# Kernel optimization log

Hardware: AMD Instinct MI355X
Metric: run time of the kernel (lower is better)

The kernel has to match this reference:

```python
import jax, jax.numpy as jnp
import numpy as np

N = 2048  # device_num
K = 32    # neighbors per device


def setup_inputs() -> dict:
    key = jax.random.key(0)
    k1, k2, k3 = jax.random.split(key, 3)
    dynamic_re = jax.random.uniform(k1, (N, N), dtype=jnp.float32)
    static_re = jax.random.uniform(k2, (N,), dtype=jnp.float32)
    # neighbor ids in [0, N) excluding self (draw in [0, N-1) then shift past row index)
    r = jax.random.randint(k3, (N, K), 0, N - 1)
    rows = jnp.arange(N)[:, None]
    neighbor_matrix = (r + (r >= rows)).astype(jnp.int32)
    return {"dynamic_re": dynamic_re, "static_re": static_re, "neighbor_matrix": neighbor_matrix}


def _trust_forward(dynamic_re, static_re, neighbor_matrix):
    # Semantics of RobustTrustComputing.__call__ on a fresh instance (temp_storage empty):
    #  - diagonal: 1.0
    #  - neighbor (j in nbr(i)): history has len 1 -> CI branch is False -> combined
    #    tau = 0.7*dyn[i,j] + 0.3*stat[j]; prev==combined -> hysteresis takes the
    #    'x <= prev' path: sigmoid(combined + 0.5) with sigmoid(z)=(1-e^-z)/(1+e^-z)=tanh(z/2)
    #  - non-neighbor with common neighbors c: 0.8 * mean_c rep[i,c]*rep[c,j] read from the
    #    PARTIALLY-FILLED matrix in row-major write order (rep[i,c] nonzero only if c<j,
    #    rep[c,j] nonzero only if c<i); divisor is the FULL common-neighbor count.
    #  - non-neighbor, no common neighbors: 0.5*stat[j]
    #  - final clamp to [0,1]
    n = dynamic_re.shape[0]
    idx = jnp.arange(n)
    # membership matrix: M[i, c] True iff c appears in neighbor list of i
    M = jnp.zeros((n, n), dtype=bool).at[idx[:, None], neighbor_matrix].set(True)
    nbrval = jnp.tanh(0.5 * (0.7 * dynamic_re + 0.3 * static_re[None, :] + 0.5))
    Mf = M.astype(dynamic_re.dtype)
    count = Mf @ Mf.T                                  # |common neighbors(i, j)|
    Bmask = Mf.T * (idx[:, None] < idx[None, :])       # [c, j]: c in nbr(j) AND c < j
    fallback = 0.5 * static_re                         # [j]

    def step(rep, xs):
        i, M_i, nbr_i, cnt_i = xs
        # rep[i, c] (c in nbr(i)) equals nbrval[i, c] once column c has been written (c < j,
        # handled by Bmask); rep[c, j] is the final row c only for c < i (rows >= i are zero).
        A = jnp.where(M_i & (idx < i), nbr_i, 0.0)     # [c]
        num = jnp.einsum('c,cj,cj->j', A, rep, Bmask)  # [j]
        indirect = 0.8 * num / jnp.maximum(cnt_i, 1.0)
        row = jnp.where(M_i, nbr_i, jnp.where(cnt_i > 0, indirect, fallback))
        row = jnp.where(idx == i, 1.0, row)            # diagonal overrides everything
        return rep.at[i].set(row), None

    rep0 = jnp.zeros((n, n), dynamic_re.dtype)
    rep, _ = jax.lax.scan(step, rep0, (idx, M, nbrval, count))
    return jnp.clip(rep, 0.0, 1.0)


def reference(dynamic_re, static_re, neighbor_matrix):
    return _trust_forward(dynamic_re, static_re, neighbor_matrix)
```

## Files before the change

### kernel.cpp

```cpp
#include <hip/hip_runtime.h>
#include <math.h>
#include <limits.h>

#define WAVE 64
#define KMAX 32
#define IMAX 96

__device__ __forceinline__ float nvval(float d, float s) {
    return tanhf(0.5f * (0.7f * d + 0.3f * s + 0.5f));
}
__device__ __forceinline__ float clamp01(float x) {
    return fminf(fmaxf(x, 0.0f), 1.0f);
}

__global__ void build_lists(const int* __restrict__ nbr, int N, int K, int W,
                            int* __restrict__ nbrs_sorted, int* __restrict__ deg,
                            unsigned* __restrict__ Mbits, unsigned* __restrict__ Tbits,
                            int* __restrict__ invcnt, int* __restrict__ invlist,
                            int* __restrict__ invpos) {
    int tid = blockIdx.x * blockDim.x + threadIdx.x;
    int i = tid / WAVE;
    int lane = tid % WAVE;
    if (i >= N) return;
    bool have = (lane < K);
    int val = have ? nbr[(size_t)i * K + lane] : INT_MAX;
    bool dup = false;
    for (int t = 0; t < K; ++t) {
        int vt = __shfl(val, t);
        if (have && t < lane && vt == val) dup = true;
    }
    int dupi = (dup || !have) ? 1 : 0;
    int pos = 0;
    for (int t = 0; t < K; ++t) {
        int vt = __shfl(val, t);
        int dt = __shfl(dupi, t);
        if (!dt && vt < val) pos++;
    }
    int myp = (have && !dup) ? pos : -1;
    unsigned long long m = __ballot(have && !dup);
    int degv = __popcll(m);
    int slot = INT_MAX;
    for (int t = 0; t < K; ++t) {
        int pt = __shfl(myp, t);
        int vt = __shfl(val, t);
        if (pt == lane) slot = vt;
    }
    if (lane < K) nbrs_sorted[(size_t)i * K + lane] = slot;
    if (lane == 0) deg[i] = degv;
    if (have) {
        atomicOr(&Mbits[(size_t)i * W + (val >> 5)], 1u << (val & 31));
        atomicOr(&Tbits[(size_t)val * W + (i >> 5)], 1u << (i & 31));
        if (!dup) {
            int p = atomicAdd(&invcnt[val], 1);
            if (p < IMAX) invlist[(size_t)val * IMAX + p] = i;
            invpos[(size_t)i * K + myp] = p;
        }
    }
}

__global__ void __launch_bounds__(256) phase1(
        const float* __restrict__ dyn, const float* __restrict__ stat,
        const int* __restrict__ nbrs_sorted, const int* __restrict__ deg,
        const unsigned* __restrict__ Mbits, const unsigned* __restrict__ Tbits,
        const int* __restrict__ invpos, int N, int K, int W,
        float* __restrict__ Vcomp) {
    __shared__ float s_nv[4 * KMAX * KMAX];
    int tid = blockIdx.x * blockDim.x + threadIdx.x;
    int j = tid / WAVE;
    int lane = threadIdx.x & (WAVE - 1);
    int waveid = threadIdx.x >> 6;
    if (j >= N) return;
    int degj = deg[j];
    int c = (lane < K) ? nbrs_sorted[(size_t)j * K + lane] : INT_MAX;
    bool validk = (lane < degj);
    float sk = validk ? stat[c] : 0.0f;
    float statj = stat[j];
    float* s_row = &s_nv[waveid * KMAX * KMAX];

    unsigned dirbit = 0;
    if (validk) {
        unsigned w = Tbits[(size_t)j * W + (c >> 5)];
        dirbit = (w >> (c & 31)) & 1u;
    }
    unsigned dirmask = (unsigned)__ballot(dirbit != 0);
    float dv = 0.0f;
    if (dirbit) dv = nvval(dyn[(size_t)c * N + j], statj);

    unsigned hmAll = 0;
    #pragma unroll
    for (int m = 0; m < KMAX; ++m) {
        int cm = __shfl(c, m);
        if (cm < N) {
            unsigned w = validk ? Mbits[(size_t)cm * W + (c >> 5)] : 0u;
            unsigned b = (w >> (c & 31)) & 1u;
            hmAll |= b << m;
            if (b && lane < m && c < j)
                s_row[m * KMAX + lane] = nvval(dyn[(size_t)cm * N + c], sk);
        }
    }
    unsigned lm = (lane < 31) ? (0xFFFFFFFEu << lane) : 0u;
    unsigned hmTerm = (validk && c < j) ? (hmAll & lm) : 0u;

    int mycnt = 0;
    unsigned H = 0;
    #pragma unroll
    for (int m = 0; m < KMAX; ++m) {
        unsigned long long ball = __ballot((hmAll >> m) & 1u);
        unsigned long long ballT = __ballot((hmTerm >> m) & 1u);
        if (lane == m) mycnt = __popcll(ball);
        H |= (ballT ? 1u : 0u) << m;
    }
    H = __builtin_amdgcn_readfirstlane(H);
    dirmask = __builtin_amdgcn_readfirstlane(dirmask);

    float v = 0.0f;
    #pragma unroll
    for (int m = 0; m < KMAX; ++m) {
        float num = 0.0f;
        if (H & (1u << m)) {
            float t = 0.0f;
            if ((hmTerm >> m) & 1u) t = s_row[m * KMAX + lane] * v;
            num = t;
            num += __shfl_xor(num, 16);
            num += __shfl_xor(num, 8);
            num += __shfl_xor(num, 4);
            num += __shfl_xor(num, 2);
            num += __shfl_xor(num, 1);
        }
        float val;
        if ((dirmask >> m) & 1u) val = dv;
        else if (mycnt > 0) val = 0.8f * num / (float)mycnt;
        else val = 0.5f * statj;
        val = clamp01(val);
        if (lane == m) v = val;
    }
    if (validk) {
        int p = invpos[(size_t)j * K + lane];
        if (p < IMAX) Vcomp[(size_t)c * IMAX + p] = v;
    }
}

__global__ void __launch_bounds__(256) phase2(
        const float* __restrict__ dyn, const float* __restrict__ stat,
        const int* __restrict__ nbrs_sorted,
        const int* __restrict__ invcnt, const int* __restrict__ invlist,
        const float* __restrict__ Vcomp,
        int N, int K, float* __restrict__ out) {
    extern __shared__ char smem[];
    int* s_cnt = (int*)smem;
    float* s_num = (float*)(s_cnt + N);
    int* s_nbr = (int*)(s_num + N);
    float* s_nv = (float*)(s_nbr + K);
    int* s_icnt = (int*)(s_nv + K);
    __shared__ int s_me;

    int i = blockIdx.x;
    int tid = threadIdx.x;

    for (int t = tid; t < N; t += blockDim.x) { s_cnt[t] = 0; s_num[t] = 0.0f; }
    if (tid < K) {
        int c = nbrs_sorted[(size_t)i * K + tid];
        s_nbr[tid] = c;
        if (c < N) {
            s_nv[tid] = nvval(dyn[(size_t)i * N + c], stat[c]);
            int m = invcnt[c];
            s_icnt[tid] = (m < IMAX) ? m : IMAX;
        } else {
            s_nv[tid] = 0.0f;
            s_icnt[tid] = 0;
        }
    }
    if (tid == 0) {
        int m = invcnt[i];
        s_me = (m < IMAX) ? m : IMAX;
    }
    __syncthreads();

    {
        int k = tid >> 3;
        int e0 = tid & 7;
        if (k < K) {
            int c = s_nbr[k];
            int m = s_icnt[k];
            float nv = s_nv[k];
            if (c < N) {
                for (int e = e0; e < m; e += 8) {
                    int j = invlist[(size_t)c * IMAX + e];
                    atomicAdd(&s_cnt[j], 1);
                    if (c < i && c < j)
                        atomicAdd(&s_num[j], nv * Vcomp[(size_t)c * IMAX + e]);
                }
            }
        }
    }
    __syncthreads();

    if (tid < K) {
        int c = s_nbr[tid];
        if (c < N) { s_cnt[c] = -1; s_num[c] = s_nv[tid]; }
    }
    __syncthreads();

    for (int e = tid; e < s_me; e += blockDim.x) {
        int j = invlist[(size_t)i * IMAX + e];
        s_cnt[j] = -1;
        s_num[j] = Vcomp[(size_t)i * IMAX + e];
    }
    __syncthreads();

    for (int j = tid; j < N; j += blockDim.x) {
        int cnt = s_cnt[j];
        float val;
        if (j == i) val = 1.0f;
        else if (cnt < 0) val = s_num[j];
        else if (cnt > 0) val = 0.8f * s_num[j] / (float)cnt;
        else val = 0.5f * stat[j];
        out[(size_t)i * N + j] = clamp01(val);
    }
}

extern "C" void kernel_launch(void* const* d_in, const int* in_sizes, int n_in,
                              void* d_out, int out_size, void* d_ws, size_t ws_size,
                              hipStream_t stream) {
    const float* dyn = (const float*)d_in[0];
    const float* stat = (const float*)d_in[1];
    const int* nbr = (const int*)d_in[2];
    int N = in_sizes[1];
    int K = in_sizes[2] / N;
    int W = (N + 31) / 32;
    float* out = (float*)d_out;

    char* ws = (char*)d_ws;
    size_t offNbr = 0;
    size_t offDeg = offNbr + (size_t)N * K * sizeof(int);
    size_t offM = offDeg + (size_t)N * sizeof(int);
    size_t offT = offM + (size_t)N * W * sizeof(unsigned);
    size_t offIC = offT + (size_t)N * W * sizeof(unsigned);
    size_t offIP = offIC + (size_t)N * sizeof(int);
    size_t offIL = offIP + (size_t)N * K * sizeof(int);
    size_t offVC = offIL + (size_t)N * IMAX * sizeof(int);
    int* nbrs_sorted = (int*)(ws + offNbr);
    int* deg = (int*)(ws + offDeg);
    unsigned* Mbits = (unsigned*)(ws + offM);
    unsigned* Tbits = (unsigned*)(ws + offT);
    int* invcnt = (int*)(ws + offIC);
    int* invpos = (int*)(ws + offIP);
    int* invlist = (int*)(ws + offIL);
    float* Vcomp = (float*)(ws + offVC);

    hipMemsetAsync(ws + offM, 0, offIP - offM, stream);

    int threads = 256;
    int blocksWave = (N * WAVE + threads - 1) / threads;
    build_lists<<<blocksWave, threads, 0, stream>>>(nbr, N, K, W, nbrs_sorted, deg,
                                                    Mbits, Tbits, invcnt, invlist,
                                                    invpos);
    phase1<<<blocksWave, threads, 0, stream>>>(dyn, stat, nbrs_sorted, deg,
                                               Mbits, Tbits, invpos, N, K, W, Vcomp);
    size_t smem = (size_t)N * 8 + (size_t)K * 12 + 16;
    phase2<<<N, threads, smem, stream>>>(dyn, stat, nbrs_sorted,
                                         invcnt, invlist, Vcomp, N, K, out);
}
```

Measured before the change: 125.0 us.

## Fuse three kernels into one persistent kernel with software grid barriers

Replaces the build_lists, phase1 and phase2 launches, plus the large memset, with a single persistent kernel of 512 blocks. It zeroes the bitmaps in-kernel and separates the phases with atomic-counter grid barriers. Each block handles 4 rows per phase, so launch gaps and inter-kernel idle time go away. In exchange the kernel depends on all 512 blocks being co-resident (launch bounds allow 2 per CU) to avoid deadlock. Phase 2 also has less parallelism, because each block now processes 4 rows in sequence instead of one block per row.

```diff
diff --git a/kernel.cpp b/kernel.cpp
--- a/kernel.cpp
+++ b/kernel.cpp
@@ -5,6 +5,8 @@
 #define WAVE 64
 #define KMAX 32
 #define IMAX 96
+#define NBLK 512
+#define TPB  256
 
 __device__ __forceinline__ float nvval(float d, float s) {
     return tanhf(0.5f * (0.7f * d + 0.3f * s + 0.5f));
@@ -13,209 +15,226 @@
     return fminf(fmaxf(x, 0.0f), 1.0f);
 }
 
-__global__ void build_lists(const int* __restrict__ nbr, int N, int K, int W,
-                            int* __restrict__ nbrs_sorted, int* __restrict__ deg,
-                            unsigned* __restrict__ Mbits, unsigned* __restrict__ Tbits,
-                            int* __restrict__ invcnt, int* __restrict__ invlist,
-                            int* __restrict__ invpos) {
-    int tid = blockIdx.x * blockDim.x + threadIdx.x;
-    int i = tid / WAVE;
-    int lane = tid % WAVE;
-    if (i >= N) return;
-    bool have = (lane < K);
-    int val = have ? nbr[(size_t)i * K + lane] : INT_MAX;
-    bool dup = false;
-    for (int t = 0; t < K; ++t) {
-        int vt = __shfl(val, t);
-        if (have && t < lane && vt == val) dup = true;
-    }
-    int dupi = (dup || !have) ? 1 : 0;
-    int pos = 0;
-    for (int t = 0; t < K; ++t) {
-        int vt = __shfl(val, t);
-        int dt = __shfl(dupi, t);
-        if (!dt && vt < val) pos++;
-    }
-    int myp = (have && !dup) ? pos : -1;
-    unsigned long long m = __ballot(have && !dup);
-    int degv = __popcll(m);
-    int slot = INT_MAX;
-    for (int t = 0; t < K; ++t) {
-        int pt = __shfl(myp, t);
-        int vt = __shfl(val, t);
-        if (pt == lane) slot = vt;
-    }
-    if (lane < K) nbrs_sorted[(size_t)i * K + lane] = slot;
-    if (lane == 0) deg[i] = degv;
-    if (have) {
-        atomicOr(&Mbits[(size_t)i * W + (val >> 5)], 1u << (val & 31));
-        atomicOr(&Tbits[(size_t)val * W + (i >> 5)], 1u << (i & 31));
-        if (!dup) {
-            int p = atomicAdd(&invcnt[val], 1);
-            if (p < IMAX) invlist[(size_t)val * IMAX + p] = i;
-            invpos[(size_t)i * K + myp] = p;
-        }
-    }
-}
-
-__global__ void __launch_bounds__(256) phase1(
+__device__ __forceinline__ void grid_sync(unsigned* bar) {
+    __threadfence();
+    __syncthreads();
+    if (threadIdx.x == 0) {
+        __hip_atomic_fetch_add(bar, 1u, __ATOMIC_ACQ_REL, __HIP_MEMORY_SCOPE_AGENT);
+        while (__hip_atomic_load(bar, __ATOMIC_ACQUIRE, __HIP_MEMORY_SCOPE_AGENT) < (unsigned)NBLK)
+            __builtin_amdgcn_s_sleep(8);
+    }
+    __syncthreads();
+    __threadfence();
+}
+
+__global__ void __launch_bounds__(TPB, 2) fused(
         const float* __restrict__ dyn, const float* __restrict__ stat,
-        const int* __restrict__ nbrs_sorted, const int* __restrict__ deg,
-        const unsigned* __restrict__ Mbits, const unsigned* __restrict__ Tbits,
-        const int* __restrict__ invpos, int N, int K, int W,
-        float* __restrict__ Vcomp) {
-    __shared__ float s_nv[4 * KMAX * KMAX];
-    int tid = blockIdx.x * blockDim.x + threadIdx.x;
-    int j = tid / WAVE;
-    int lane = threadIdx.x & (WAVE - 1);
-    int waveid = threadIdx.x >> 6;
-    if (j >= N) return;
-    int degj = deg[j];
-    int c = (lane < K) ? nbrs_sorted[(size_t)j * K + lane] : INT_MAX;
-    bool validk = (lane < degj);
-    float sk = validk ? stat[c] : 0.0f;
-    float statj = stat[j];
-    float* s_row = &s_nv[waveid * KMAX * KMAX];
-
-    unsigned dirbit = 0;
-    if (validk) {
-        unsigned w = Tbits[(size_t)j * W + (c >> 5)];
-        dirbit = (w >> (c & 31)) & 1u;
-    }
-    unsigned dirmask = (unsigned)__ballot(dirbit != 0);
-    float dv = 0.0f;
-    if (dirbit) dv = nvval(dyn[(size_t)c * N + j], statj);
-
-    unsigned hmAll = 0;
-    #pragma unroll
-    for (int m = 0; m < KMAX; ++m) {
-        int cm = __shfl(c, m);
-        if (cm < N) {
-            unsigned w = validk ? Mbits[(size_t)cm * W + (c >> 5)] : 0u;
-            unsigned b = (w >> (c & 31)) & 1u;
-            hmAll |= b << m;
-            if (b && lane < m && c < j)
-                s_row[m * KMAX + lane] = nvval(dyn[(size_t)cm * N + c], sk);
-        }
-    }
-    unsigned lm = (lane < 31) ? (0xFFFFFFFEu << lane) : 0u;
-    unsigned hmTerm = (validk && c < j) ? (hmAll & lm) : 0u;
-
-    int mycnt = 0;
-    unsigned H = 0;
-    #pragma unroll
-    for (int m = 0; m < KMAX; ++m) {
-        unsigned long long ball = __ballot((hmAll >> m) & 1u);
-        unsigned long long ballT = __ballot((hmTerm >> m) & 1u);
-        if (lane == m) mycnt = __popcll(ball);
-        H |= (ballT ? 1u : 0u) << m;
-    }
-    H = __builtin_amdgcn_readfirstlane(H);
-    dirmask = __builtin_amdgcn_readfirstlane(dirmask);
-
-    float v = 0.0f;
-    #pragma unroll
-    for (int m = 0; m < KMAX; ++m) {
-        float num = 0.0f;
-        if (H & (1u << m)) {
-            float t = 0.0f;
-            if ((hmTerm >> m) & 1u) t = s_row[m * KMAX + lane] * v;
-            num = t;
-            num += __shfl_xor(num, 16);
-            num += __shfl_xor(num, 8);
-            num += __shfl_xor(num, 4);
-            num += __shfl_xor(num, 2);
-            num += __shfl_xor(num, 1);
-        }
-        float val;
-        if ((dirmask >> m) & 1u) val = dv;
-        else if (mycnt > 0) val = 0.8f * num / (float)mycnt;
-        else val = 0.5f * statj;
-        val = clamp01(val);
-        if (lane == m) v = val;
-    }
-    if (validk) {
-        int p = invpos[(size_t)j * K + lane];
-        if (p < IMAX) Vcomp[(size_t)c * IMAX + p] = v;
-    }
-}
-
-__global__ void __launch_bounds__(256) phase2(
-        const float* __restrict__ dyn, const float* __restrict__ stat,
-        const int* __restrict__ nbrs_sorted,
-        const int* __restrict__ invcnt, const int* __restrict__ invlist,
-        const float* __restrict__ Vcomp,
-        int N, int K, float* __restrict__ out) {
-    extern __shared__ char smem[];
-    int* s_cnt = (int*)smem;
-    float* s_num = (float*)(s_cnt + N);
-    int* s_nbr = (int*)(s_num + N);
-    float* s_nv = (float*)(s_nbr + K);
-    int* s_icnt = (int*)(s_nv + K);
-    __shared__ int s_me;
-
-    int i = blockIdx.x;
+        const int* __restrict__ nbr, int N, int K, int W,
+        unsigned* __restrict__ Mbits, unsigned* __restrict__ Tbits,
+        int* __restrict__ invcnt, unsigned* __restrict__ bars,
+        int* __restrict__ invpos, int* __restrict__ invlist,
+        float* __restrict__ Vcomp, int* __restrict__ nbrs_sorted,
+        int* __restrict__ deg, float* __restrict__ out) {
+    __shared__ __align__(16) char smem[17 * 1024];
     int tid = threadIdx.x;
-
-    for (int t = tid; t < N; t += blockDim.x) { s_cnt[t] = 0; s_num[t] = 0.0f; }
-    if (tid < K) {
-        int c = nbrs_sorted[(size_t)i * K + tid];
-        s_nbr[tid] = c;
-        if (c < N) {
-            s_nv[tid] = nvval(dyn[(size_t)i * N + c], stat[c]);
-            int m = invcnt[c];
-            s_icnt[tid] = (m < IMAX) ? m : IMAX;
-        } else {
-            s_nv[tid] = 0.0f;
-            s_icnt[tid] = 0;
-        }
-    }
-    if (tid == 0) {
-        int m = invcnt[i];
-        s_me = (m < IMAX) ? m : IMAX;
-    }
-    __syncthreads();
+    int lane = tid & (WAVE - 1);
+    int wid = tid >> 6;
+    int row = blockIdx.x * 4 + wid;
 
     {
-        int k = tid >> 3;
-        int e0 = tid & 7;
-        if (k < K) {
-            int c = s_nbr[k];
-            int m = s_icnt[k];
-            float nv = s_nv[k];
-            if (c < N) {
-                for (int e = e0; e < m; e += 8) {
-                    int j = invlist[(size_t)c * IMAX + e];
-                    atomicAdd(&s_cnt[j], 1);
-                    if (c < i && c < j)
-                        atomicAdd(&s_num[j], nv * Vcomp[(size_t)c * IMAX + e]);
+        size_t zwords = (size_t)N * W * 2 + N;
+        unsigned* zb = Mbits;
+        for (size_t t = (size_t)blockIdx.x * TPB + tid; t < zwords; t += (size_t)NBLK * TPB)
+            zb[t] = 0u;
+    }
+    grid_sync(&bars[0]);
+
+    if (row < N) {
+        int i = row;
+        bool have = (lane < K);
+        int val = have ? nbr[(size_t)i * K + lane] : INT_MAX;
+        bool dup = false;
+        for (int t = 0; t < KMAX; ++t) {
+            int vt = __shfl(val, t);
+            if (have && t < lane && vt == val) dup = true;
+        }
+        int dupi = (dup || !have) ? 1 : 0;
+        int pos = 0;
+        for (int t = 0; t < KMAX; ++t) {
+            int vt = __shfl(val, t);
+            int dt = __shfl(dupi, t);
+            if (!dt && vt < val) pos++;
+        }
+        int myp = (have && !dup) ? pos : -1;
+        unsigned long long m = __ballot(have && !dup);
+        int degv = __popcll(m);
+        int slot = INT_MAX;
+        for (int t = 0; t < KMAX; ++t) {
+            int pt = __shfl(myp, t);
+            int vt = __shfl(val, t);
+            if (pt == lane) slot = vt;
+        }
+        if (lane < K) nbrs_sorted[(size_t)i * K + lane] = slot;
+        if (lane == 0) deg[i] = degv;
+        if (have) {
+            atomicOr(&Mbits[(size_t)i * W + (val >> 5)], 1u << (val & 31));
+            atomicOr(&Tbits[(size_t)val * W + (i >> 5)], 1u << (i & 31));
+            if (!dup) {
+                int p = atomicAdd(&invcnt[val], 1);
+                if (p < IMAX) invlist[(size_t)val * IMAX + p] = i;
+                invpos[(size_t)i * K + myp] = p;
+            }
+        }
+    }
+    grid_sync(&bars[1]);
+
+    if (row < N) {
+        int j = row;
+        float* s_row = (float*)smem + (size_t)wid * KMAX * KMAX;
+        int degj = deg[j];
+        int c = (lane < K) ? nbrs_sorted[(size_t)j * K + lane] : INT_MAX;
+        bool validk = (lane < degj);
+        float sk = validk ? stat[c] : 0.0f;
+        float statj = stat[j];
+
+        unsigned dirbit = 0;
+        if (validk) {
+            unsigned w = Tbits[(size_t)j * W + (c >> 5)];
+            dirbit = (w >> (c & 31)) & 1u;
+        }
+        unsigned dirmask = (unsigned)__ballot(dirbit != 0);
+        float dv = 0.0f;
+        if (dirbit) dv = nvval(dyn[(size_t)c * N + j], statj);
+
+        unsigned hmAll = 0;
+        #pragma unroll
+        for (int m = 0; m < KMAX; ++m) {
+            int cm = __shfl(c, m);
+            if (cm < N) {
+                unsigned w = validk ? Mbits[(size_t)cm * W + (c >> 5)] : 0u;
+                unsigned b = (w >> (c & 31)) & 1u;
+                hmAll |= b << m;
+                if (b && lane < m && c < j)
+                    s_row[m * KMAX + lane] = nvval(dyn[(size_t)cm * N + c], sk);
+            }
+        }
+        unsigned lm = (lane < 31) ? (0xFFFFFFFEu << lane) : 0u;
+        unsigned hmTerm = (validk && c < j) ? (hmAll & lm) : 0u;
+
+        int mycnt = 0;
+        unsigned H = 0;
+        #pragma unroll
+        for (int m = 0; m < KMAX; ++m) {
+            unsigned long long ball = __ballot((hmAll >> m) & 1u);
+            unsigned long long ballT = __ballot((hmTerm >> m) & 1u);
+            if (lane == m) mycnt = __popcll(ball);
+            H |= (ballT ? 1u : 0u) << m;
+        }
+        H = __builtin_amdgcn_readfirstlane(H);
+        dirmask = __builtin_amdgcn_readfirstlane(dirmask);
+
+        float v = 0.0f;
+        #pragma unroll
+        for (int m = 0; m < KMAX; ++m) {
+            float num = 0.0f;
+            if (H & (1u << m)) {
+                float t = 0.0f;
+                if ((hmTerm >> m) & 1u) t = s_row[m * KMAX + lane] * v;
+                num = t;
+                num += __shfl_xor(num, 16);
+                num += __shfl_xor(num, 8);
+                num += __shfl_xor(num, 4);
+                num += __shfl_xor(num, 2);
+                num += __shfl_xor(num, 1);
+            }
+            float val;
+            if ((dirmask >> m) & 1u) val = dv;
+            else if (mycnt > 0) val = 0.8f * num / (float)mycnt;
+            else val = 0.5f * statj;
+            val = clamp01(val);
+            if (lane == m) v = val;
+        }
+        if (validk) {
+            int p = invpos[(size_t)j * K + lane];
+            if (p < IMAX) Vcomp[(size_t)c * IMAX + p] = v;
+        }
+    }
+    grid_sync(&bars[2]);
+
+    {
+        int* s_cnt = (int*)smem;
+        float* s_num = (float*)(s_cnt + N);
+        int* s_nbr = (int*)(s_num + N);
+        float* s_nv = (float*)(s_nbr + KMAX);
+        int* s_icnt = (int*)(s_nv + KMAX);
+        int* s_me = (int*)(s_icnt + KMAX);
+
+        for (int r = 0; r < 4; ++r) {
+            int i = blockIdx.x * 4 + r;
+            if (i >= N) break;
+            __syncthreads();
+            for (int t = tid; t < N; t += TPB) { s_cnt[t] = 0; s_num[t] = 0.0f; }
+            if (tid < K) {
+                int c = nbrs_sorted[(size_t)i * K + tid];
+                s_nbr[tid] = c;
+                if (c < N) {
+                    s_nv[tid] = nvval(dyn[(size_t)i * N + c], stat[c]);
+                    int m = invcnt[c];
+                    s_icnt[tid] = (m < IMAX) ? m : IMAX;
+                } else {
+                    s_nv[tid] = 0.0f;
+                    s_icnt[tid] = 0;
                 }
             }
-        }
-    }
-    __syncthreads();
-
-    if (tid < K) {
-        int c = s_nbr[tid];
-        if (c < N) { s_cnt[c] = -1; s_num[c] = s_nv[tid]; }
-    }
-    __syncthreads();
-
-    for (int e = tid; e < s_me; e += blockDim.x) {
-        int j = invlist[(size_t)i * IMAX + e];
-        s_cnt[j] = -1;
-        s_num[j] = Vcomp[(size_t)i * IMAX + e];
-    }
-    __syncthreads();
-
-    for (int j = tid; j < N; j += blockDim.x) {
-        int cnt = s_cnt[j];
-        float val;
-        if (j == i) val = 1.0f;
-        else if (cnt < 0) val = s_num[j];
-        else if (cnt > 0) val = 0.8f * s_num[j] / (float)cnt;
-        else val = 0.5f * stat[j];
-        out[(size_t)i * N + j] = clamp01(val);
+            if (tid == 0) {
+                int m = invcnt[i];
+                *s_me = (m < IMAX) ? m : IMAX;
+            }
+            __syncthreads();
+
+            {
+                int k = tid >> 3;
+                int e0 = tid & 7;
+                if (k < K) {
+                    int c = s_nbr[k];
+                    int m = s_icnt[k];
+                    float nv = s_nv[k];
+                    if (c < N) {
+                        for (int e = e0; e < m; e += 8) {
+                            int j = invlist[(size_t)c * IMAX + e];
+                            atomicAdd(&s_cnt[j], 1);
+                            if (c < i && c < j)
+                                atomicAdd(&s_num[j], nv * Vcomp[(size_t)c * IMAX + e]);
+                        }
+                    }
+                }
+            }
+            __syncthreads();
+
+            if (tid < K) {
+                int c = s_nbr[tid];
+                if (c < N) { s_cnt[c] = -1; s_num[c] = s_nv[tid]; }
+            }
+            __syncthreads();
+
+            int me = *s_me;
+            for (int e = tid; e < me; e += TPB) {
+                int j = invlist[(size_t)i * IMAX + e];
+                s_cnt[j] = -1;
+                s_num[j] = Vcomp[(size_t)i * IMAX + e];
+            }
+            __syncthreads();
+
+            for (int j = tid; j < N; j += TPB) {
+                int cnt = s_cnt[j];
+                float val;
+                if (j == i) val = 1.0f;
+                else if (cnt < 0) val = s_num[j];
+                else if (cnt > 0) val = 0.8f * s_num[j] / (float)cnt;
+                else val = 0.5f * stat[j];
+                out[(size_t)i * N + j] = clamp01(val);
+            }
+        }
     }
 }
 
@@ -231,33 +250,28 @@
     float* out = (float*)d_out;
 
     char* ws = (char*)d_ws;
-    size_t offNbr = 0;
-    size_t offDeg = offNbr + (size_t)N * K * sizeof(int);
-    size_t offM = offDeg + (size_t)N * sizeof(int);
+    size_t offM = 0;
     size_t offT = offM + (size_t)N * W * sizeof(unsigned);
     size_t offIC = offT + (size_t)N * W * sizeof(unsigned);
-    size_t offIP = offIC + (size_t)N * sizeof(int);
+    size_t offBar = offIC + (size_t)N * sizeof(int);
+    size_t offIP = offBar + 64;
     size_t offIL = offIP + (size_t)N * K * sizeof(int);
     size_t offVC = offIL + (size_t)N * IMAX * sizeof(int);
-    int* nbrs_sorted = (int*)(ws + offNbr);
-    int* deg = (int*)(ws + offDeg);
+    size_t offNbr = offVC + (size_t)N * IMAX * sizeof(float);
+    size_t offDeg = offNbr + (size_t)N * K * sizeof(int);
     unsigned* Mbits = (unsigned*)(ws + offM);
     unsigned* Tbits = (unsigned*)(ws + offT);
     int* invcnt = (int*)(ws + offIC);
+    unsigned* bars = (unsigned*)(ws + offBar);
     int* invpos = (int*)(ws + offIP);
     int* invlist = (int*)(ws + offIL);
     float* Vcomp = (float*)(ws + offVC);
-
-    hipMemsetAsync(ws + offM, 0, offIP - offM, stream);
-
-    int threads = 256;
-    int blocksWave = (N * WAVE + threads - 1) / threads;
-    build_lists<<<blocksWave, threads, 0, stream>>>(nbr, N, K, W, nbrs_sorted, deg,
-                                                    Mbits, Tbits, invcnt, invlist,
-                                                    invpos);
-    phase1<<<blocksWave, threads, 0, stream>>>(dyn, stat, nbrs_sorted, deg,
-                                               Mbits, Tbits, invpos, N, K, W, Vcomp);
-    size_t smem = (size_t)N * 8 + (size_t)K * 12 + 16;
-    phase2<<<N, threads, smem, stream>>>(dyn, stat, nbrs_sorted,
-                                         invcnt, invlist, Vcomp, N, K, out);
-}
+    int* nbrs_sorted = (int*)(ws + offNbr);
+    int* deg = (int*)(ws + offDeg);
+
+    hipMemsetAsync(ws + offBar, 0, 64, stream);
+
+    fused<<<NBLK, TPB, 0, stream>>>(dyn, stat, nbr, N, K, W,
+                                    Mbits, Tbits, invcnt, bars,
+                                    invpos, invlist, Vcomp, nbrs_sorted, deg, out);
+}
```

Result: slower. 429.4 us (+243.6%).

## Drop transposed bitmask, build membership bits without atomics, vectorize phase2 reads

Applied to the files above, without the earlier changes.

Removes the Tbits transposed membership bitmap. Phase1 now tests direct membership by reading Mbits[c] at bit j. Each lane builds one Mbits word from wave shuffles and writes it directly, which removes the global atomicOr traffic and shrinks the workspace memset to just invcnt. Phase2 reads the inverse lists and Vcomp with int4/float4 loads, and tanh is replaced by an exp-based formula. The lane-per-word Mbits build assumes W fits in one 64-lane wave (N ≤ 2048), and the fast exp path slightly changes numerics.

```diff
diff --git a/kernel.cpp b/kernel.cpp
--- a/kernel.cpp
+++ b/kernel.cpp
@@ -7,7 +7,9 @@
 #define IMAX 96
 
 __device__ __forceinline__ float nvval(float d, float s) {
-    return tanhf(0.5f * (0.7f * d + 0.3f * s + 0.5f));
+    float z = 0.7f * d + 0.3f * s + 0.5f;
+    float e = __expf(z);
+    return 1.0f - 2.0f / (e + 1.0f);
 }
 __device__ __forceinline__ float clamp01(float x) {
     return fminf(fmaxf(x, 0.0f), 1.0f);
@@ -15,7 +17,7 @@
 
 __global__ void build_lists(const int* __restrict__ nbr, int N, int K, int W,
                             int* __restrict__ nbrs_sorted, int* __restrict__ deg,
-                            unsigned* __restrict__ Mbits, unsigned* __restrict__ Tbits,
+                            unsigned* __restrict__ Mbits,
                             int* __restrict__ invcnt, int* __restrict__ invlist,
                             int* __restrict__ invpos) {
     int tid = blockIdx.x * blockDim.x + threadIdx.x;
@@ -25,13 +27,18 @@
     bool have = (lane < K);
     int val = have ? nbr[(size_t)i * K + lane] : INT_MAX;
     bool dup = false;
-    for (int t = 0; t < K; ++t) {
+    unsigned mybits = 0;
+    #pragma unroll
+    for (int t = 0; t < KMAX; ++t) {
         int vt = __shfl(val, t);
         if (have && t < lane && vt == val) dup = true;
-    }
+        if ((vt >> 5) == lane) mybits |= 1u << (vt & 31);
+    }
+    if (lane < W) Mbits[(size_t)i * W + lane] = mybits;
     int dupi = (dup || !have) ? 1 : 0;
     int pos = 0;
-    for (int t = 0; t < K; ++t) {
+    #pragma unroll
+    for (int t = 0; t < KMAX; ++t) {
         int vt = __shfl(val, t);
         int dt = __shfl(dupi, t);
         if (!dt && vt < val) pos++;
@@ -40,28 +47,25 @@
     unsigned long long m = __ballot(have && !dup);
     int degv = __popcll(m);
     int slot = INT_MAX;
-    for (int t = 0; t < K; ++t) {
+    #pragma unroll
+    for (int t = 0; t < KMAX; ++t) {
         int pt = __shfl(myp, t);
         int vt = __shfl(val, t);
         if (pt == lane) slot = vt;
     }
     if (lane < K) nbrs_sorted[(size_t)i * K + lane] = slot;
     if (lane == 0) deg[i] = degv;
-    if (have) {
-        atomicOr(&Mbits[(size_t)i * W + (val >> 5)], 1u << (val & 31));
-        atomicOr(&Tbits[(size_t)val * W + (i >> 5)], 1u << (i & 31));
-        if (!dup) {
-            int p = atomicAdd(&invcnt[val], 1);
-            if (p < IMAX) invlist[(size_t)val * IMAX + p] = i;
-            invpos[(size_t)i * K + myp] = p;
-        }
+    if (have && !dup) {
+        int p = atomicAdd(&invcnt[val], 1);
+        if (p < IMAX) invlist[(size_t)val * IMAX + p] = i;
+        invpos[(size_t)i * K + myp] = p;
     }
 }
 
 __global__ void __launch_bounds__(256) phase1(
         const float* __restrict__ dyn, const float* __restrict__ stat,
         const int* __restrict__ nbrs_sorted, const int* __restrict__ deg,
-        const unsigned* __restrict__ Mbits, const unsigned* __restrict__ Tbits,
+        const unsigned* __restrict__ Mbits,
         const int* __restrict__ invpos, int N, int K, int W,
         float* __restrict__ Vcomp) {
     __shared__ float s_nv[4 * KMAX * KMAX];
@@ -79,8 +83,8 @@
 
     unsigned dirbit = 0;
     if (validk) {
-        unsigned w = Tbits[(size_t)j * W + (c >> 5)];
-        dirbit = (w >> (c & 31)) & 1u;
+        unsigned w = Mbits[(size_t)c * W + (j >> 5)];
+        dirbit = (w >> (j & 31)) & 1u;
     }
     unsigned dirmask = (unsigned)__ballot(dirbit != 0);
     float dv = 0.0f;
@@ -150,8 +154,8 @@
     int* s_cnt = (int*)smem;
     float* s_num = (float*)(s_cnt + N);
     int* s_nbr = (int*)(s_num + N);
-    float* s_nv = (float*)(s_nbr + K);
-    int* s_icnt = (int*)(s_nv + K);
+    float* s_nv = (float*)(s_nbr + KMAX);
+    int* s_icnt = (int*)(s_nv + KMAX);
     __shared__ int s_me;
 
     int i = blockIdx.x;
@@ -178,17 +182,29 @@
 
     {
         int k = tid >> 3;
-        int e0 = tid & 7;
+        int sub = tid & 7;
         if (k < K) {
             int c = s_nbr[k];
             int m = s_icnt[k];
             float nv = s_nv[k];
             if (c < N) {
-                for (int e = e0; e < m; e += 8) {
-                    int j = invlist[(size_t)c * IMAX + e];
-                    atomicAdd(&s_cnt[j], 1);
-                    if (c < i && c < j)
-                        atomicAdd(&s_num[j], nv * Vcomp[(size_t)c * IMAX + e]);
+                const int4* il4 = (const int4*)&invlist[(size_t)c * IMAX];
+                const float4* vc4 = (const float4*)&Vcomp[(size_t)c * IMAX];
+                for (int base = sub * 4; base < m; base += 32) {
+                    int4 js = il4[base >> 2];
+                    float4 vs = vc4[base >> 2];
+                    int jj[4] = {js.x, js.y, js.z, js.w};
+                    float vv[4] = {vs.x, vs.y, vs.z, vs.w};
+                    #pragma unroll
+                    for (int t = 0; t < 4; ++t) {
+                        int e = base + t;
+                        if (e < m) {
+                            int j = jj[t];
+                            atomicAdd(&s_cnt[j], 1);
+                            if (c < i && c < j)
+                                atomicAdd(&s_num[j], nv * vv[t]);
+                        }
+                    }
                 }
             }
         }
@@ -201,7 +217,8 @@
     }
     __syncthreads();
 
-    for (int e = tid; e < s_me; e += blockDim.x) {
+    int me = s_me;
+    for (int e = tid; e < me; e += blockDim.x) {
         int j = invlist[(size_t)i * IMAX + e];
         s_cnt[j] = -1;
         s_num[j] = Vcomp[(size_t)i * IMAX + e];
@@ -231,33 +248,30 @@
     float* out = (float*)d_out;
 
     char* ws = (char*)d_ws;
-    size_t offNbr = 0;
-    size_t offDeg = offNbr + (size_t)N * K * sizeof(int);
-    size_t offM = offDeg + (size_t)N * sizeof(int);
-    size_t offT = offM + (size_t)N * W * sizeof(unsigned);
-    size_t offIC = offT + (size_t)N * W * sizeof(unsigned);
-    size_t offIP = offIC + (size_t)N * sizeof(int);
+    size_t offIC = 0;
+    size_t offM = offIC + (size_t)N * sizeof(int);
+    size_t offIP = offM + (size_t)N * W * sizeof(unsigned);
     size_t offIL = offIP + (size_t)N * K * sizeof(int);
     size_t offVC = offIL + (size_t)N * IMAX * sizeof(int);
-    int* nbrs_sorted = (int*)(ws + offNbr);
-    int* deg = (int*)(ws + offDeg);
+    size_t offNbr = offVC + (size_t)N * IMAX * sizeof(float);
+    size_t offDeg = offNbr + (size_t)N * K * sizeof(int);
+    int* invcnt = (int*)(ws + offIC);
     unsigned* Mbits = (unsigned*)(ws + offM);
-    unsigned* Tbits = (unsigned*)(ws + offT);
-    int* invcnt = (int*)(ws + offIC);
     int* invpos = (int*)(ws + offIP);
     int* invlist = (int*)(ws + offIL);
     float* Vcomp = (float*)(ws + offVC);
-
-    hipMemsetAsync(ws + offM, 0, offIP - offM, stream);
+    int* nbrs_sorted = (int*)(ws + offNbr);
+    int* deg = (int*)(ws + offDeg);
+
+    hipMemsetAsync(ws + offIC, 0, (size_t)N * sizeof(int), stream);
 
     int threads = 256;
     int blocksWave = (N * WAVE + threads - 1) / threads;
     build_lists<<<blocksWave, threads, 0, stream>>>(nbr, N, K, W, nbrs_sorted, deg,
-                                                    Mbits, Tbits, invcnt, invlist,
-                                                    invpos);
+                                                    Mbits, invcnt, invlist, invpos);
     phase1<<<blocksWave, threads, 0, stream>>>(dyn, stat, nbrs_sorted, deg,
-                                               Mbits, Tbits, invpos, N, K, W, Vcomp);
-    size_t smem = (size_t)N * 8 + (size_t)K * 12 + 16;
+                                               Mbits, invpos, N, K, W, Vcomp);
+    size_t smem = (size_t)N * 8 + (size_t)KMAX * 12 + 16;
     phase2<<<N, threads, smem, stream>>>(dyn, stat, nbrs_sorted,
                                          invcnt, invlist, Vcomp, N, K, out);
 }
```

Result: faster. 115.2 us (-7.8%).
